# Kernel optimization log

Measured on AMD Instinct MI355X. Metric: run time of the kernel, lower is better.

Reference implementation:

```python
import jax, jax.numpy as jnp
import numpy as np
from jax.scipy.special import logsumexp

B, N, F_IN, HID = 8, 1024, 256, 128
RATIO = 0.5
NUM_LAYERS = 2
EPS_OT = 0.01  # forward default epsilon


def setup_inputs():
    key = jax.random.key(0)
    ks = jax.random.split(key, 6)
    x = jax.random.normal(ks[0], (B, N, F_IN), dtype=jnp.float32)
    adj = (jax.random.uniform(ks[1], (B, N, N)) < 0.02).astype(jnp.float32)
    adj = jnp.maximum(adj, jnp.swapaxes(adj, 1, 2))  # symmetric sparse-ish graph
    mask = jnp.ones((B, N), dtype=bool)
    W1 = jax.random.normal(ks[2], (F_IN, HID), dtype=jnp.float32) / np.sqrt(F_IN)
    b1 = jnp.zeros((HID,), dtype=jnp.float32)
    Watt = jax.random.normal(ks[3], (HID, 1), dtype=jnp.float32) / np.sqrt(HID)
    batt = jnp.zeros((1,), dtype=jnp.float32)
    W2 = jax.random.normal(ks[4], (HID, F_IN), dtype=jnp.float32) / np.sqrt(HID)
    b2 = jnp.zeros((F_IN,), dtype=jnp.float32)
    return dict(x=x, adj=adj, mask=mask, W1=W1, b1=b1, Watt=Watt, batt=batt,
                W2=W2, b2=b2, opt_epochs=20)


def _gcn_norm(adj):
    # DenseGCNConv add_loop + symmetric normalization
    n = adj.shape[-1]
    A = adj + jnp.eye(n, dtype=adj.dtype)
    d = jnp.maximum(A.sum(-1), 1.0) ** -0.5
    return d[..., :, None] * A * d[..., None, :]


def dense_gcn(x, adj, W, b, mask=None):
    out = jnp.einsum('bij,bjh->bih', _gcn_norm(adj), x @ W) + b
    if mask is not None:
        out = out * mask[..., None].astype(out.dtype)
    return out


def normalize_batch_adj(adj):
    # CoarsenBlock.normalize_batch_adj: self-loop sym-norm, zero-row masked
    n = adj.shape[-1]
    A = adj + jnp.eye(n, dtype=adj.dtype)
    d = jnp.maximum(A.sum(-1), 1.0) ** -0.5
    newA = d[..., :, None] * A * d[..., None, :]
    return (adj.sum(-1) > 0).astype(adj.dtype)[..., None] * newA


def coarsen_block(x, adj, Watt, batt):
    # attention score per node, squared then sigmoid  -> [B, N]
    alpha = jax.nn.sigmoid(dense_gcn(x, adj, Watt, batt) ** 2)[..., 0]
    norm_adj = normalize_batch_adj(adj)
    k = int(adj.shape[1] * RATIO) + 1
    cut = jax.lax.top_k(alpha, k)[0][:, -1]                 # per-sample k-th value
    cut_alpha = jax.nn.relu(alpha + 1e-7 - cut[:, None])    # soft top-k gate
    S = norm_adj * cut_alpha[:, None, :]
    S = S / jnp.maximum(jnp.abs(S).sum(-1, keepdims=True), 1e-12)  # row L1 norm
    emb = jnp.einsum('bij,bif->bjf', S, x)                  # S^T x
    tmp = jnp.einsum('bij,bik->bjk', S, adj)                # S^T adj
    new_adj = jnp.einsum('bjk,bkl->bjl', tmp, S)            # S^T adj S
    return emb, new_adj, S


def sinkhorn_loss(x, y, eps, niter):
    # squared-euclidean cost via gram trick (no [n,m,f] intermediate)
    C = (jnp.sum(x * x, -1)[:, None] + jnp.sum(y * y, -1)[None, :]
         - 2.0 * (x @ y.T))
    n, m = C.shape
    log_mu = jnp.full((n,), -np.log(n), dtype=C.dtype)
    log_nu = jnp.full((m,), -np.log(m), dtype=C.dtype)

    def M(u, v):
        return (-C + u[:, None] + v[None, :]) / eps

    def step(carry, _):
        u, v = carry
        u = eps * (log_mu - logsumexp(M(u, v), axis=1)) + u
        v = eps * (log_nu - logsumexp(M(u, v), axis=0)) + v
        return (u, v), None

    (u, v), _ = jax.lax.scan(step, (jnp.zeros_like(log_mu), jnp.zeros_like(log_nu)),
                             None, length=niter)
    pi = jnp.exp(M(u, v))
    return jnp.sum(pi * C)


def reference(x, adj, mask, W1, b1, Watt, batt, W2, b2, opt_epochs):
    x1 = jax.nn.relu(dense_gcn(x, adj, W1, b1, mask))
    xs0 = x1.mean(axis=1)
    new_adjs = [adj]
    Ss = []
    coarse_x, new_adj = x1, adj
    for _ in range(NUM_LAYERS):
        coarse_x, new_adj, S = coarsen_block(coarse_x, new_adj, Watt, batt)
        new_adjs.append(new_adj)
        Ss.append(S)
    x2 = dense_gcn(coarse_x, new_adj, W2, b2, mask)
    xs1 = x2.mean(axis=1)
    loss_fn = lambda a, b: sinkhorn_loss(a, b, EPS_OT, opt_epochs)
    opt_loss = jnp.sum(jax.vmap(loss_fn)(x, x2))
    return (xs0, xs1, new_adjs[0], new_adjs[1], new_adjs[2], Ss[0], Ss[1], opt_loss)
```

## Files before the change

kernel.cpp:

```cpp
#include <hip/hip_runtime.h>
#include <math.h>

#define BN   8
#define NN   1024
#define FIN  256
#define HIDN 128
#define KTOP 513
#define NITER 20
#define EPS_S 0.01f
#define INV_EPS 100.0f
#define LOG_MU (-6.9314718055994531f)
#define SNB 256
#define SENTU 0xFFFFFFFFu

typedef __attribute__((ext_vector_type(8))) short bfrag8;
typedef __attribute__((ext_vector_type(4))) float facc4;

#define GLOAD16(g, l) __builtin_amdgcn_global_load_lds( \
    (const __attribute__((address_space(1))) unsigned int*)(g), \
    (__attribute__((address_space(3))) unsigned int*)(l), 16, 0, 0)

static __device__ __forceinline__ float wred_sum(float s) {
#pragma unroll
  for (int o = 32; o > 0; o >>= 1) s += __shfl_xor(s, o);
  return s;
}
static __device__ __forceinline__ unsigned short f2b(float f) {
  unsigned int u = __float_as_uint(f);
  u += 0x7fff + ((u >> 16) & 1);
  return (unsigned short)(u >> 16);
}
static __device__ __forceinline__ float b2f(unsigned short h) {
  return __uint_as_float((unsigned int)h << 16);
}

template<int WRBF, int WCOPY>
__global__ __launch_bounds__(256) void k_rowstats4(const float* __restrict__ adj,
                                                   float* __restrict__ dv,
                                                   float* __restrict__ rm,
                                                   unsigned short* __restrict__ abf,
                                                   float* __restrict__ ocopy) {
  int r0 = blockIdx.x << 2;
  int t = threadIdx.x, lane = t & 63, wv = t >> 6;
  __shared__ float sm[4][4];
#pragma unroll
  for (int r = 0; r < 4; ++r) {
    float4 v = ((const float4*)(adj + (long)(r0 + r) * NN))[t];
    if (WRBF) {
      ushort4 h; h.x = f2b(v.x); h.y = f2b(v.y); h.z = f2b(v.z); h.w = f2b(v.w);
      *(ushort4*)(abf + (long)(r0 + r) * NN + t * 4) = h;
    }
    if (WCOPY) ((float4*)(ocopy + (long)(r0 + r) * NN))[t] = v;
    float s = (v.x + v.y) + (v.z + v.w);
    s = wred_sum(s);
    if (lane == 0) sm[wv][r] = s;
  }
  __syncthreads();
  if (t < 4) {
    float tot = sm[0][t] + sm[1][t] + sm[2][t] + sm[3][t];
    dv[r0 + t] = rsqrtf(fmaxf(tot + 1.0f, 1.0f));
    rm[r0 + t] = tot > 0.0f ? 1.0f : 0.0f;
  }
}

__global__ __launch_bounds__(256) void k_rowstats4b(
    const unsigned short* __restrict__ abf, float* __restrict__ dv,
    float* __restrict__ rm) {
  int r0 = blockIdx.x << 2;
  int t = threadIdx.x, lane = t & 63, wv = t >> 6;
  __shared__ float sm[4][4];
#pragma unroll
  for (int r = 0; r < 4; ++r) {
    ushort4 h = ((const ushort4*)(abf + (long)(r0 + r) * NN))[t];
    float s = (b2f(h.x) + b2f(h.y)) + (b2f(h.z) + b2f(h.w));
    s = wred_sum(s);
    if (lane == 0) sm[wv][r] = s;
  }
  __syncthreads();
  if (t < 4) {
    float tot = sm[0][t] + sm[1][t] + sm[2][t] + sm[3][t];
    dv[r0 + t] = rsqrtf(fmaxf(tot + 1.0f, 1.0f));
    rm[r0 + t] = tot > 0.0f ? 1.0f : 0.0f;
  }
}

__global__ __launch_bounds__(256) void k_f2b(const float* __restrict__ X,
                                             unsigned short* __restrict__ Y) {
  long i = ((long)blockIdx.x * 256 + threadIdx.x) * 4;
  float4 v = *(const float4*)(X + i);
  Y[i] = f2b(v.x); Y[i + 1] = f2b(v.y); Y[i + 2] = f2b(v.z); Y[i + 3] = f2b(v.w);
}

__global__ __launch_bounds__(256) void k_w1t(const float* __restrict__ W,
                                             unsigned short* __restrict__ Wt) {
  int idx = blockIdx.x * 256 + threadIdx.x;
  int n = idx >> 8, k = idx & 255;
  Wt[idx] = f2b(W[k * HIDN + n]);
}

__global__ __launch_bounds__(256) void k_prep2(
    const float* __restrict__ X0, const float* __restrict__ X1,
    unsigned short* __restrict__ Xh0, unsigned short* __restrict__ Xl0,
    unsigned short* __restrict__ Xh1, unsigned short* __restrict__ Xl1,
    float* __restrict__ sq0, float* __restrict__ sq1) {
  int bb = blockIdx.x;
  const float* X; unsigned short* Xh; unsigned short* Xl; float* sq; int rb;
  if (bb < 2048) { X = X0; Xh = Xh0; Xl = Xl0; sq = sq0; rb = bb; }
  else { X = X1; Xh = Xh1; Xl = Xl1; sq = sq1; rb = bb - 2048; }
  int t = threadIdx.x, lane = t & 63, wv = t >> 6;
  int row = rb * 4 + wv;
  long base = (long)row * FIN + lane * 4;
  float4 v = *(const float4*)(X + base);
  ushort4 h, l;
  h.x = f2b(v.x); l.x = f2b(v.x - b2f(h.x));
  h.y = f2b(v.y); l.y = f2b(v.y - b2f(h.y));
  h.z = f2b(v.z); l.z = f2b(v.z - b2f(h.z));
  h.w = f2b(v.w); l.w = f2b(v.w - b2f(h.w));
  *(ushort4*)(Xh + base) = h;
  *(ushort4*)(Xl + base) = l;
  float s = v.x * v.x + v.y * v.y + v.z * v.z + v.w * v.w;
  s = wred_sum(s);
  if (lane == 0) sq[row] = s;
}

__global__ __launch_bounds__(256) void k_transp(const float* __restrict__ X,
                                                unsigned short* __restrict__ Xt,
                                                int R, int C) {
  __shared__ float tile[64][65];
  long bb = blockIdx.z;
  const float* Xb = X + bb * (long)R * C;
  unsigned short* Xtb = Xt + bb * (long)R * C;
  int r0 = blockIdx.y * 64, c0 = blockIdx.x * 64;
  int t = threadIdx.x;
  int tr = t >> 4, tc4 = (t & 15) * 4;
#pragma unroll
  for (int p = 0; p < 4; ++p) {
    float4 v = *(const float4*)(Xb + (long)(r0 + tr + p * 16) * C + c0 + tc4);
    tile[tr + p * 16][tc4 + 0] = v.x; tile[tr + p * 16][tc4 + 1] = v.y;
    tile[tr + p * 16][tc4 + 2] = v.z; tile[tr + p * 16][tc4 + 3] = v.w;
  }
  __syncthreads();
  int jj = t >> 2, i0 = (t & 3) * 16;
  unsigned short* orow = Xtb + (long)(c0 + jj) * R + r0 + i0;
#pragma unroll
  for (int q = 0; q < 16; ++q) orow[q] = f2b(tile[i0 + q][jj]);
}

template<int SPLIT>
__global__ __launch_bounds__(256) void k_stc(const float* __restrict__ XW,
                                             const float* __restrict__ dvv,
                                             unsigned short* __restrict__ Bh,
                                             unsigned short* __restrict__ Bl,
                                             int F) {
  __shared__ float tile[64][65];
  __shared__ float dl[64];
  int bz = blockIdx.z;
  const float* Xb = XW + (long)bz * NN * F;
  int j0 = blockIdx.x * 64;
  int n0 = blockIdx.y * 64;
  int t = threadIdx.x;
  int tr = t >> 4, tc4 = (t & 15) * 4;
#pragma unroll
  for (int p = 0; p < 4; ++p) {
    float4 v = *(const float4*)(Xb + (long)(j0 + tr + p * 16) * F + n0 + tc4);
    tile[tr + p * 16][tc4 + 0] = v.x; tile[tr + p * 16][tc4 + 1] = v.y;
    tile[tr + p * 16][tc4 + 2] = v.z; tile[tr + p * 16][tc4 + 3] = v.w;
  }
  if (t < 64) dl[t] = dvv[(bz << 10) + j0 + t];
  __syncthreads();
  int nn = t >> 2, i0 = (t & 3) * 16;
  long obase = ((long)bz * F + n0 + nn) * NN + j0 + i0;
#pragma unroll
  for (int q = 0; q < 16; ++q) {
    float v = tile[i0 + q][nn] * dl[i0 + q];
    unsigned short h = f2b(v);
    Bh[obase + q] = h;
    if (SPLIT) Bl[obase + q] = f2b(v - b2f(h));
  }
}

template<int WF32, int WBF>
__global__ __launch_bounds__(256) void k_mfma_nt(
    const unsigned short* __restrict__ A, const unsigned short* __restrict__ B,
    float* __restrict__ Cf, unsigned short* __restrict__ Cb,
    unsigned short* __restrict__ Cb2,
    int K, int ldA, int ldB, int ldC, long sA, long sB, long sC) {
  __shared__ unsigned short As[128 * 32];
  __shared__ unsigned short Bs[128 * 32];
  int bz = blockIdx.z;
  A += bz * sA; B += bz * sB;
  int m0 = blockIdx.y * 128, n0 = blockIdx.x * 128;
  int tid = threadIdx.x, lane = tid & 63, w = tid >> 6;
  int wr = w >> 1, wc = w & 1;
  facc4 acc[4][4];
#pragma unroll
  for (int i = 0; i < 4; ++i)
#pragma unroll
    for (int j = 0; j < 4; ++j)
#pragma unroll
      for (int q = 0; q < 4; ++q) acc[i][j][q] = 0.f;

  int rA0 = w * 16 + (lane >> 2);
  int kslot = lane & 3;

  for (int k0 = 0; k0 < K; k0 += 32) {
#pragma unroll
    for (int i = 0; i < 2; ++i) {
      int row = i * 64 + rA0;
      int ks = (kslot ^ (row & 3)) << 3;
      GLOAD16(A + (long)(m0 + row) * ldA + k0 + ks, As + (i * 64 + w * 16) * 32);
      GLOAD16(B + (long)(n0 + row) * ldB + k0 + ks, Bs + (i * 64 + w * 16) * 32);
    }
    __syncthreads();
    bfrag8 af[4], bfr[4];
#pragma unroll
    for (int mi = 0; mi < 4; ++mi) {
      int row = wr * 64 + mi * 16 + (lane & 15);
      int sl = (((lane >> 4) ^ (row & 3)) << 3);
      af[mi] = *(const bfrag8*)(As + row * 32 + sl);
    }
#pragma unroll
    for (int ni = 0; ni < 4; ++ni) {
      int row = wc * 64 + ni * 16 + (lane & 15);
      int sl = (((lane >> 4) ^ (row & 3)) << 3);
      bfr[ni] = *(const bfrag8*)(Bs + row * 32 + sl);
    }
#pragma unroll
    for (int mi = 0; mi < 4; ++mi)
#pragma unroll
      for (int ni = 0; ni < 4; ++ni)
        acc[mi][ni] = __builtin_amdgcn_mfma_f32_16x16x32_bf16(
            af[mi], bfr[ni], acc[mi][ni], 0, 0, 0);
    __syncthreads();
  }
  if (WF32) Cf += bz * sC;
  if (WBF) Cb += bz * sC;
  if (WBF == 2) Cb2 += bz * sC;
#pragma unroll
  for (int mi = 0; mi < 4; ++mi) {
    int rowb = m0 + wr * 64 + mi * 16 + ((lane >> 4) << 2);
#pragma unroll
    for (int ni = 0; ni < 4; ++ni) {
      int col = n0 + wc * 64 + ni * 16 + (lane & 15);
#pragma unroll
      for (int q = 0; q < 4; ++q) {
        long off = (long)(rowb + q) * ldC + col;
        float v = acc[mi][ni][q];
        if (WF32) Cf[off] = v;
        if (WBF == 1) Cb[off] = f2b(v);
        if (WBF == 2) {
          unsigned short h = f2b(v);
          Cb[off] = h;
          Cb2[off] = f2b(v - b2f(h));
        }
      }
    }
  }
}

__global__ __launch_bounds__(256) void k_coars(
    const unsigned short* __restrict__ St, const unsigned short* __restrict__ Badj,
    const unsigned short* __restrict__ cxt,
    unsigned short* __restrict__ tmpo, float* __restrict__ embo) {
  __shared__ unsigned short As[128 * 32];
  __shared__ unsigned short Bs[128 * 32];
  int bz = blockIdx.z;
  int bx = blockIdx.x;
  int em = (bx == 8);
  const unsigned short* A = St + (long)bz * 1048576;
  const unsigned short* B = em ? (cxt + (long)bz * 131072)
                               : (Badj + (long)bz * 1048576);
  int m0 = blockIdx.y * 128, n0 = em ? 0 : bx * 128;
  int tid = threadIdx.x, lane = tid & 63, w = tid >> 6;
  int wr = w >> 1, wc = w & 1;
  facc4 acc[4][4];
#pragma unroll
  for (int i = 0; i < 4; ++i)
#pragma unroll
    for (int j = 0; j < 4; ++j)
#pragma unroll
      for (int q = 0; q < 4; ++q) acc[i][j][q] = 0.f;

  int rA0 = w * 16 + (lane >> 2);
  int kslot = lane & 3;

  for (int k0 = 0; k0 < NN; k0 += 32) {
#pragma unroll
    for (int i = 0; i < 2; ++i) {
      int row = i * 64 + rA0;
      int ks = (kslot ^ (row & 3)) << 3;
      GLOAD16(A + (long)(m0 + row) * NN + k0 + ks, As + (i * 64 + w * 16) * 32);
      GLOAD16(B + (long)(n0 + row) * NN + k0 + ks, Bs + (i * 64 + w * 16) * 32);
    }
    __syncthreads();
    bfrag8 af[4], bfr[4];
#pragma unroll
    for (int mi = 0; mi < 4; ++mi) {
      int row = wr * 64 + mi * 16 + (lane & 15);
      int sl = (((lane >> 4) ^ (row & 3)) << 3);
      af[mi] = *(const bfrag8*)(As + row * 32 + sl);
    }
#pragma unroll
    for (int ni = 0; ni < 4; ++ni) {
      int row = wc * 64 + ni * 16 + (lane & 15);
      int sl = (((lane >> 4) ^ (row & 3)) << 3);
      bfr[ni] = *(const bfrag8*)(Bs + row * 32 + sl);
    }
#pragma unroll
    for (int mi = 0; mi < 4; ++mi)
#pragma unroll
      for (int ni = 0; ni < 4; ++ni)
        acc[mi][ni] = __builtin_amdgcn_mfma_f32_16x16x32_bf16(
            af[mi], bfr[ni], acc[mi][ni], 0, 0, 0);
    __syncthreads();
  }
#pragma unroll
  for (int mi = 0; mi < 4; ++mi) {
    int rowb = m0 + wr * 64 + mi * 16 + ((lane >> 4) << 2);
#pragma unroll
    for (int ni = 0; ni < 4; ++ni) {
      int col = n0 + wc * 64 + ni * 16 + (lane & 15);
#pragma unroll
      for (int q = 0; q < 4; ++q) {
        float v = acc[mi][ni][q];
        if (em)
          embo[(long)bz * 131072 + (long)(rowb + q) * HIDN + col] = v;
        else
          tmpo[(long)bz * 1048576 + (long)(rowb + q) * NN + col] = f2b(v);
      }
    }
  }
}

template<int SPLIT, int RELU>
__global__ __launch_bounds__(256) void k_mfma_gcn(
    const unsigned short* __restrict__ Ah, const unsigned short* __restrict__ Al,
    const unsigned short* __restrict__ Bh, const unsigned short* __restrict__ Bl,
    const float* __restrict__ dvv, const float* __restrict__ XW,
    const float* __restrict__ bias, float* __restrict__ Cf, int F) {
  __shared__ unsigned short AsH[128 * 32], BsH[128 * 32];
  __shared__ unsigned short AsL[SPLIT ? 128 * 32 : 16], BsL[SPLIT ? 128 * 32 : 16];
  int bz = blockIdx.z;
  const unsigned short* Ahb = Ah + (long)bz * NN * NN;
  const unsigned short* Alb = SPLIT ? Al + (long)bz * NN * NN : nullptr;
  const unsigned short* Bhb = Bh + (long)bz * F * NN;
  const unsigned short* Blb = SPLIT ? Bl + (long)bz * F * NN : nullptr;
  int m0 = blockIdx.y * 128, n0 = blockIdx.x * 128;
  int tid = threadIdx.x, lane = tid & 63, w = tid >> 6;
  int wr = w >> 1, wc = w & 1;
  facc4 acc[4][4];
#pragma unroll
  for (int i = 0; i < 4; ++i)
#pragma unroll
    for (int j = 0; j < 4; ++j)
#pragma unroll
      for (int q = 0; q < 4; ++q) acc[i][j][q] = 0.f;

  int rA0 = w * 16 + (lane >> 2);
  int kslot = lane & 3;

  for (int k0 = 0; k0 < NN; k0 += 32) {
#pragma unroll
    for (int i = 0; i < 2; ++i) {
      int row = i * 64 + rA0;
      int ks = (kslot ^ (row & 3)) << 3;
      int ld = (i * 64 + w * 16) * 32;
      GLOAD16(Ahb + (long)(m0 + row) * NN + k0 + ks, AsH + ld);
      GLOAD16(Bhb + (long)(n0 + row) * NN + k0 + ks, BsH + ld);
      if (SPLIT) {
        GLOAD16(Alb + (long)(m0 + row) * NN + k0 + ks, AsL + ld);
        GLOAD16(Blb + (long)(n0 + row) * NN + k0 + ks, BsL + ld);
      }
    }
    __syncthreads();
    bfrag8 afh[4], bfh[4], afl[4], bfl[4];
#pragma unroll
    for (int mi = 0; mi < 4; ++mi) {
      int row = wr * 64 + mi * 16 + (lane & 15);
      int sl = (((lane >> 4) ^ (row & 3)) << 3);
      afh[mi] = *(const bfrag8*)(AsH + row * 32 + sl);
      if (SPLIT) afl[mi] = *(const bfrag8*)(AsL + row * 32 + sl);
    }
#pragma unroll
    for (int ni = 0; ni < 4; ++ni) {
      int row = wc * 64 + ni * 16 + (lane & 15);
      int sl = (((lane >> 4) ^ (row & 3)) << 3);
      bfh[ni] = *(const bfrag8*)(BsH + row * 32 + sl);
      if (SPLIT) bfl[ni] = *(const bfrag8*)(BsL + row * 32 + sl);
    }
#pragma unroll
    for (int mi = 0; mi < 4; ++mi)
#pragma unroll
      for (int ni = 0; ni < 4; ++ni) {
        acc[mi][ni] = __builtin_amdgcn_mfma_f32_16x16x32_bf16(
            afh[mi], bfh[ni], acc[mi][ni], 0, 0, 0);
        if (SPLIT) {
          acc[mi][ni] = __builtin_amdgcn_mfma_f32_16x16x32_bf16(
              afh[mi], bfl[ni], acc[mi][ni], 0, 0, 0);
          acc[mi][ni] = __builtin_amdgcn_mfma_f32_16x16x32_bf16(
              afl[mi], bfh[ni], acc[mi][ni], 0, 0, 0);
        }
      }
    __syncthreads();
  }
  Cf += (long)bz * NN * F;
#pragma unroll
  for (int mi = 0; mi < 4; ++mi) {
    int rowb = m0 + wr * 64 + mi * 16 + ((lane >> 4) << 2);
#pragma unroll
    for (int ni = 0; ni < 4; ++ni) {
      int col = n0 + wc * 64 + ni * 16 + (lane & 15);
      float bcol = bias[col];
#pragma unroll
      for (int q = 0; q < 4; ++q) {
        float dm = dvv[(bz << 10) + rowb + q];
        float xwv = XW[((long)(bz << 10) + rowb + q) * F + col];
        float v = dm * (acc[mi][ni][q] + dm * xwv) + bcol;
        if (RELU) v = fmaxf(v, 0.f);
        Cf[(long)(rowb + q) * F + col] = v;
      }
    }
  }
}

__global__ __launch_bounds__(256) void k_mfma_gram(
    const unsigned short* __restrict__ Ah, const unsigned short* __restrict__ Al,
    const unsigned short* __restrict__ Bh, const unsigned short* __restrict__ Bl,
    const float* __restrict__ xx, const float* __restrict__ yy,
    float* __restrict__ Cf, float* __restrict__ Ct) {
  __shared__ unsigned short AsH[128 * 32], AsL[128 * 32];
  __shared__ unsigned short BsH[128 * 32], BsL[128 * 32];
  int bz = blockIdx.z;
  long boff = (long)bz * NN * FIN;
  Ah += boff; Al += boff; Bh += boff; Bl += boff;
  const float* xxb = xx + (bz << 10);
  const float* yyb = yy + (bz << 10);
  int m0 = blockIdx.y * 128, n0 = blockIdx.x * 128;
  int tid = threadIdx.x, lane = tid & 63, w = tid >> 6;
  int wr = w >> 1, wc = w & 1;
  facc4 acc[4][4];
#pragma unroll
  for (int i = 0; i < 4; ++i)
#pragma unroll
    for (int j = 0; j < 4; ++j)
#pragma unroll
      for (int q = 0; q < 4; ++q) acc[i][j][q] = 0.f;

  int rA0 = w * 16 + (lane >> 2);
  int kslot = lane & 3;

  for (int k0 = 0; k0 < FIN; k0 += 32) {
#pragma unroll
    for (int i = 0; i < 2; ++i) {
      int row = i * 64 + rA0;
      int ks = (kslot ^ (row & 3)) << 3;
      long ga = (long)(m0 + row) * FIN + k0 + ks;
      long gb = (long)(n0 + row) * FIN + k0 + ks;
      int ld = (i * 64 + w * 16) * 32;
      GLOAD16(Ah + ga, AsH + ld);
      GLOAD16(Al + ga, AsL + ld);
      GLOAD16(Bh + gb, BsH + ld);
      GLOAD16(Bl + gb, BsL + ld);
    }
    __syncthreads();
    bfrag8 afh[4], afl[4], bfh[4], bfl[4];
#pragma unroll
    for (int mi = 0; mi < 4; ++mi) {
      int row = wr * 64 + mi * 16 + (lane & 15);
      int sl = (((lane >> 4) ^ (row & 3)) << 3);
      afh[mi] = *(const bfrag8*)(AsH + row * 32 + sl);
      afl[mi] = *(const bfrag8*)(AsL + row * 32 + sl);
    }
#pragma unroll
    for (int ni = 0; ni < 4; ++ni) {
      int row = wc * 64 + ni * 16 + (lane & 15);
      int sl = (((lane >> 4) ^ (row & 3)) << 3);
      bfh[ni] = *(const bfrag8*)(BsH + row * 32 + sl);
      bfl[ni] = *(const bfrag8*)(BsL + row * 32 + sl);
    }
#pragma unroll
    for (int mi = 0; mi < 4; ++mi)
#pragma unroll
      for (int ni = 0; ni < 4; ++ni) {
        acc[mi][ni] = __builtin_amdgcn_mfma_f32_16x16x32_bf16(
            afh[mi], bfh[ni], acc[mi][ni], 0, 0, 0);
        acc[mi][ni] = __builtin_amdgcn_mfma_f32_16x16x32_bf16(
            afh[mi], bfl[ni], acc[mi][ni], 0, 0, 0);
        acc[mi][ni] = __builtin_amdgcn_mfma_f32_16x16x32_bf16(
            afl[mi], bfh[ni], acc[mi][ni], 0, 0, 0);
      }
    __syncthreads();
  }
  Cf += (long)bz * NN * NN;
  Ct += (long)bz * NN * NN;
#pragma unroll
  for (int mi = 0; mi < 4; ++mi) {
    int rowb = m0 + wr * 64 + mi * 16 + ((lane >> 4) << 2);
#pragma unroll
    for (int ni = 0; ni < 4; ++ni) {
      int col = n0 + wc * 64 + ni * 16 + (lane & 15);
      float yv = yyb[col];
      float4 tv;
#pragma unroll
      for (int q = 0; q < 4; ++q) {
        float v = xxb[rowb + q] + yv - 2.f * acc[mi][ni][q];
        Cf[(long)(rowb + q) * NN + col] = v;
        ((float*)&tv)[q] = v;
      }
      *(float4*)(Ct + (long)col * NN + rowb) = tv;
    }
  }
}

__global__ __launch_bounds__(256) void k_rowdot(const float* __restrict__ X,
                                                const float* __restrict__ w,
                                                float* __restrict__ out) {
  int t = threadIdx.x; int lane = t & 63; int wv = t >> 6;
  int row = blockIdx.x * 4 + wv;
  const float* xr = X + (long)row * HIDN;
  float s = xr[lane] * w[lane] + xr[lane + 64] * w[lane + 64];
  s = wred_sum(s);
  if (lane == 0) out[row] = s;
}

__global__ __launch_bounds__(256) void k_alpha4b(const unsigned short* __restrict__ adj,
                                                 const float* __restrict__ dv,
                                                 const float* __restrict__ s0,
                                                 const float* __restrict__ batt,
                                                 float* __restrict__ alpha) {
  int r0 = blockIdx.x << 2; int b = r0 >> 10; int i0 = r0 & (NN - 1);
  int t = threadIdx.x, lane = t & 63, wv = t >> 6;
  float4 d4 = ((const float4*)(dv + (b << 10)))[t];
  float4 s4 = ((const float4*)(s0 + (b << 10)))[t];
  float w4[4];
  w4[0] = d4.x * s4.x; w4[1] = d4.y * s4.y; w4[2] = d4.z * s4.z; w4[3] = d4.w * s4.w;
  __shared__ float sm[4][4];
#pragma unroll
  for (int r = 0; r < 4; ++r) {
    ushort4 h = ((const ushort4*)(adj + (long)(r0 + r) * NN))[t];
    float dot = b2f(h.x) * w4[0] + b2f(h.y) * w4[1] +
                b2f(h.z) * w4[2] + b2f(h.w) * w4[3];
    int i = i0 + r;
    if ((i >> 2) == t) dot += w4[i & 3];
    dot = wred_sum(dot);
    if (lane == 0) sm[wv][r] = dot;
  }
  __syncthreads();
  if (t < 4) {
    float dot = sm[0][t] + sm[1][t] + sm[2][t] + sm[3][t];
    float tt = dv[r0 + t] * dot + batt[0];
    alpha[r0 + t] = 1.f / (1.f + __expf(-tt * tt));
  }
}

__global__ __launch_bounds__(512) void k_topk(const float* __restrict__ alpha,
                                              float* __restrict__ cut) {
  __shared__ float smv[NN];
  int b = blockIdx.x; int t = threadIdx.x;
  smv[t] = alpha[(b << 10) + t];
  smv[t + 512] = alpha[(b << 10) + t + 512];
  __syncthreads();
  for (int k2 = 2; k2 <= NN; k2 <<= 1) {
    for (int j2 = k2 >> 1; j2 > 0; j2 >>= 1) {
      int i = ((t / j2) * (j2 << 1)) + (t % j2);
      int ixj = i + j2;
      bool up = ((i & k2) == 0);
      float a = smv[i], c = smv[ixj];
      if ((a > c) == up) { smv[i] = c; smv[ixj] = a; }
      __syncthreads();
    }
  }
  if (t == 0) cut[b] = smv[NN - KTOP];
}

__global__ __launch_bounds__(256) void k_sbuild4b(const unsigned short* __restrict__ adj,
                                                  const float* __restrict__ dv,
                                                  const float* __restrict__ rm,
                                                  const float* __restrict__ alpha,
                                                  const float* __restrict__ cut,
                                                  float* __restrict__ S) {
  int r0 = blockIdx.x << 2; int b = r0 >> 10; int i0 = r0 & (NN - 1);
  int t = threadIdx.x, lane = t & 63, wv = t >> 6;
  float cb = cut[b];
  float4 d4 = ((const float4*)(dv + (b << 10)))[t];
  float4 al4 = ((const float4*)(alpha + (b << 10)))[t];
  float4 dg;
  dg.x = d4.x * fmaxf(al4.x + 1e-7f - cb, 0.f);
  dg.y = d4.y * fmaxf(al4.y + 1e-7f - cb, 0.f);
  dg.z = d4.z * fmaxf(al4.z + 1e-7f - cb, 0.f);
  dg.w = d4.w * fmaxf(al4.w + 1e-7f - cb, 0.f);
  __shared__ float sm[4][4];
  __shared__ float sinv[4];
  float4 vals[4];
#pragma unroll
  for (int r = 0; r < 4; ++r) {
    float di = dv[r0 + r] * rm[r0 + r];
    ushort4 h = ((const ushort4*)(adj + (long)(r0 + r) * NN))[t];
    float4 a4;
    a4.x = b2f(h.x); a4.y = b2f(h.y); a4.z = b2f(h.z); a4.w = b2f(h.w);
    int i = i0 + r;
    if ((i >> 2) == t) ((float*)&a4)[i & 3] += 1.f;
    vals[r].x = di * dg.x * a4.x; vals[r].y = di * dg.y * a4.y;
    vals[r].z = di * dg.z * a4.z; vals[r].w = di * dg.w * a4.w;
    float s = (fabsf(vals[r].x) + fabsf(vals[r].y)) +
              (fabsf(vals[r].z) + fabsf(vals[r].w));
    s = wred_sum(s);
    if (lane == 0) sm[wv][r] = s;
  }
  __syncthreads();
  if (t < 4) sinv[t] = 1.f / fmaxf(sm[0][t] + sm[1][t] + sm[2][t] + sm[3][t], 1e-12f);
  __syncthreads();
#pragma unroll
  for (int r = 0; r < 4; ++r) {
    float inv = sinv[r];
    float4 o; o.x = vals[r].x * inv; o.y = vals[r].y * inv;
    o.z = vals[r].z * inv; o.w = vals[r].w * inv;
    ((float4*)(S + (long)(r0 + r) * NN))[t] = o;
  }
}

template<int GCN>
__global__ __launch_bounds__(256) void k_gemm_ks(
    const float* __restrict__ A, const float* __restrict__ Bm, float* __restrict__ P,
    int M, int Nn, int K, int KS, long sA, long sB,
    const float* __restrict__ dv) {
  __shared__ float As[8][132];
  __shared__ float Bs[8][132];
  int z = blockIdx.z;
  int b = z / KS, ks = z % KS;
  int KC = K / KS;
  A += (long)b * sA; Bm += (long)b * sB;
  const float* dvb = GCN ? (dv + (long)b * NN) : nullptr;
  int m0 = blockIdx.y * 128, n0 = blockIdx.x * 128;
  int tid = threadIdx.x;
  int tx = tid & 15, ty = tid >> 4;
  float acc[8][8];
#pragma unroll
  for (int i = 0; i < 8; i++)
#pragma unroll
    for (int j = 0; j < 8; j++) acc[i][j] = 0.f;

  float drow = 0.f;
  if (GCN) drow = dvb[m0 + (tid >> 1)];

  for (int k0 = ks * KC; k0 < ks * KC + KC; k0 += 8) {
    {
      int r = tid >> 1, c4 = (tid & 1) * 4;
      float4 av = *(const float4*)(A + (long)(m0 + r) * K + k0 + c4);
      float a4[4] = {av.x, av.y, av.z, av.w};
      if (GCN) {
#pragma unroll
        for (int q = 0; q < 4; ++q) {
          int gj = k0 + c4 + q;
          float val = a4[q] + ((m0 + r) == gj ? 1.f : 0.f);
          a4[q] = drow * dvb[gj] * val;
        }
      }
      As[c4 + 0][r] = a4[0]; As[c4 + 1][r] = a4[1];
      As[c4 + 2][r] = a4[2]; As[c4 + 3][r] = a4[3];
    }
    {
      int kr = tid >> 5, c4 = (tid & 31) * 4;
      float4 bv = *(const float4*)(Bm + (long)(k0 + kr) * Nn + n0 + c4);
      *(float4*)&Bs[kr][c4] = bv;
    }
    __syncthreads();
#pragma unroll
    for (int k = 0; k < 8; ++k) {
      float av[8], bv[8];
      *(float4*)&av[0] = *(const float4*)&As[k][ty * 8];
      *(float4*)&av[4] = *(const float4*)&As[k][ty * 8 + 4];
      *(float4*)&bv[0] = *(const float4*)&Bs[k][tx * 8];
      *(float4*)&bv[4] = *(const float4*)&Bs[k][tx * 8 + 4];
#pragma unroll
      for (int i = 0; i < 8; i++)
#pragma unroll
        for (int j = 0; j < 8; j++)
          acc[i][j] = fmaf(av[i], bv[j], acc[i][j]);
    }
    __syncthreads();
  }
  float* Pz = P + (long)z * M * Nn;
#pragma unroll
  for (int i = 0; i < 8; ++i) {
    int m = m0 + ty * 8 + i;
    float* prow = Pz + (long)m * Nn + n0 + tx * 8;
    *(float4*)&prow[0] = *(float4*)&acc[i][0];
    *(float4*)&prow[4] = *(float4*)&acc[i][4];
  }
}

template<int RELU, int BIAS>
__global__ __launch_bounds__(256) void k_red_bias(
    const float* __restrict__ P, const float* __restrict__ bias,
    float* __restrict__ out, int Nn, int KS, long chunk) {
  long u = ((long)blockIdx.x * 256 + threadIdx.x) * 4;
  long b = u / chunk; long rem = u % chunk;
  const float* p = P + b * KS * chunk + rem;
  float4 s = *(const float4*)p;
  for (int k = 1; k < KS; ++k) {
    float4 q = *(const float4*)(p + (long)k * chunk);
    s.x += q.x; s.y += q.y; s.z += q.z; s.w += q.w;
  }
  if (BIAS) {
    int n = (int)(rem % Nn);
    s.x += bias[n]; s.y += bias[n + 1]; s.z += bias[n + 2]; s.w += bias[n + 3];
  }
  if (RELU) {
    s.x = fmaxf(s.x, 0.f); s.y = fmaxf(s.y, 0.f);
    s.z = fmaxf(s.z, 0.f); s.w = fmaxf(s.w, 0.f);
  }
  *(float4*)(out + u) = s;
}

__global__ __launch_bounds__(256) void k_colmean(const float* __restrict__ X, int Fd,
                                                 float* __restrict__ out) {
  int nb = Fd >> 6;
  int b = blockIdx.x / nb; int f0 = (blockIdx.x % nb) << 6;
  int t = threadIdx.x;
  int f = f0 + (t & 63); int rc = t >> 6;
  const float* xb = X + (long)b * NN * Fd;
  float s = 0.f;
  for (int i = rc * 256; i < rc * 256 + 256; ++i) s += xb[(long)i * Fd + f];
  __shared__ float sm[256];
  sm[t] = s; __syncthreads();
  if (t < 64) out[b * Fd + f] = (sm[t] + sm[t + 64] + sm[t + 128] + sm[t + 192]) * (1.f / NN);
}


static __device__ __forceinline__ float2 load_cohere2(const float* p) {
  float2 v;
  asm volatile("global_load_dwordx2 %0, %1, off sc0 sc1\n\ts_waitcnt vmcnt(0)"
               : "=v"(v) : "v"(p) : "memory");
  return v;
}
static __device__ __forceinline__ float load_cohere1(const float* p) {
  float v;
  asm volatile("global_load_dword %0, %1, off sc0 sc1\n\ts_waitcnt vmcnt(0)"
               : "=v"(v) : "v"(p) : "memory");
  return v;
}
static __device__ __forceinline__ void store_cohere1(float* p, float v) {
  asm volatile("global_store_dword %0, %1, off sc0 sc1\n\ts_waitcnt vmcnt(0)"
               :: "v"(p), "v"(v) : "memory");
}

static __device__ __forceinline__ void pollstage(const float* __restrict__ src,
                                                 float* __restrict__ vls, int t) {
  float2 v; int spin = 0;
  for (;;) {
    v = load_cohere2(src + t * 2);
    if ((__float_as_uint(v.x) != SENTU) & (__float_as_uint(v.y) != SENTU)) break;
    if (++spin > (1 << 20)) break;
    __builtin_amdgcn_s_sleep(1);
  }
  __syncthreads();
  *(float2*)(vls + t * 2) = v;
  __syncthreads();
}

template<int LOSS, int STORE>
static __device__ __forceinline__ void pass_reg(const float4 (&Cr)[16],
    const float* __restrict__ vls, float* __restrict__ dbout,
    int jc, int row, float* __restrict__ lossacc, float& mxs, int fresh) {
  float4 vr[16];
#pragma unroll
  for (int k = 0; k < 16; ++k)
    vr[k] = *(const float4*)(vls + (k * 16 + jc) * 4);
  float mx = mxs;
  if (fresh) {
    float m0 = -3.0e38f, m1 = m0, m2 = m0, m3 = m0;
#pragma unroll
    for (int k = 0; k < 16; ++k) {
      m0 = fmaxf(m0, vr[k].x - Cr[k].x);
      m1 = fmaxf(m1, vr[k].y - Cr[k].y);
      m2 = fmaxf(m2, vr[k].z - Cr[k].z);
      m3 = fmaxf(m3, vr[k].w - Cr[k].w);
    }
    mx = fmaxf(fmaxf(m0, m1), fmaxf(m2, m3));
#pragma unroll
    for (int m = 1; m <= 8; m <<= 1) mx = fmaxf(mx, __shfl_xor(mx, m));
  }
  float ls, ld = 0.f;
  {
    float s0 = 0, s1 = 0, s2 = 0, s3 = 0, d0 = 0, d1 = 0, d2 = 0, d3 = 0;
#pragma unroll
    for (int k = 0; k < 16; ++k) {
      float e0 = __expf(vr[k].x - Cr[k].x - mx);
      float e1 = __expf(vr[k].y - Cr[k].y - mx);
      float e2 = __expf(vr[k].z - Cr[k].z - mx);
      float e3 = __expf(vr[k].w - Cr[k].w - mx);
      s0 += e0; s1 += e1; s2 += e2; s3 += e3;
      if (LOSS) {
        d0 = fmaf(e0, Cr[k].x, d0); d1 = fmaf(e1, Cr[k].y, d1);
        d2 = fmaf(e2, Cr[k].z, d2); d3 = fmaf(e3, Cr[k].w, d3);
      }
    }
    ls = (s0 + s1) + (s2 + s3);
    if (LOSS) ld = (d0 + d1) + (d2 + d3);
  }
#pragma unroll
  for (int m = 1; m <= 8; m <<= 1) {
    ls += __shfl_xor(ls, m);
    if (LOSS) ld += __shfl_xor(ld, m);
  }
  if (!(ls > 1e-25f && ls < 1e25f)) {
    float m0 = -3.0e38f, m1 = m0, m2 = m0, m3 = m0;
#pragma unroll
    for (int k = 0; k < 16; ++k) {
      m0 = fmaxf(m0, vr[k].x - Cr[k].x);
      m1 = fmaxf(m1, vr[k].y - Cr[k].y);
      m2 = fmaxf(m2, vr[k].z - Cr[k].z);
      m3 = fmaxf(m3, vr[k].w - Cr[k].w);
    }
    mx = fmaxf(fmaxf(m0, m1), fmaxf(m2, m3));
#pragma unroll
    for (int m = 1; m <= 8; m <<= 1) mx = fmaxf(mx, __shfl_xor(mx, m));
    float s0 = 0, s1 = 0, s2 = 0, s3 = 0, d0 = 0, d1 = 0, d2 = 0, d3 = 0;
#pragma unroll
    for (int k = 0; k < 16; ++k) {
      float e0 = __expf(vr[k].x - Cr[k].x - mx);
      float e1 = __expf(vr[k].y - Cr[k].y - mx);
      float e2 = __expf(vr[k].z - Cr[k].z - mx);
      float e3 = __expf(vr[k].w - Cr[k].w - mx);
      s0 += e0; s1 += e1; s2 += e2; s3 += e3;
      if (LOSS) {
        d0 = fmaf(e0, Cr[k].x, d0); d1 = fmaf(e1, Cr[k].y, d1);
        d2 = fmaf(e2, Cr[k].z, d2); d3 = fmaf(e3, Cr[k].w, d3);
      }
    }
    ls = (s0 + s1) + (s2 + s3);
    if (LOSS) ld = (d0 + d1) + (d2 + d3);
#pragma unroll
    for (int m = 1; m <= 8; m <<= 1) {
      ls += __shfl_xor(ls, m);
      if (LOSS) ld += __shfl_xor(ld, m);
    }
  }
  mxs = mx;
  if (jc == 0) {
    float uval = LOG_MU - (mx + __logf(ls));
    if (STORE) store_cohere1(dbout + row, uval);
    if (LOSS) *lossacc += (ld / ls) * (1.0f / 1024.0f);
  }
}

__global__ __launch_bounds__(512, 1) void k_sink_reg(
    const float* __restrict__ Cm, const float* __restrict__ Ct,
    float* __restrict__ db, float* __restrict__ part,
    float* __restrict__ oloss) {
  int bid = blockIdx.x, t = threadIdx.x, lane = t & 63, wvi = t >> 6;
  int jc = lane & 15;
  int grp = bid & 7;
  int inner = bid >> 3;
  int row = (grp << 10) + inner * 32 + wvi * 4 + (lane >> 4);
  __shared__ float vls[1024];
  float4 Creg[16], Ctreg[16];
  {
    const float4* cp = (const float4*)(Cm + (long)row * NN);
    const float4* tp = (const float4*)(Ct + (long)row * NN);
#pragma unroll
    for (int k = 0; k < 16; ++k) {
      float4 c = cp[k * 16 + jc], ct = tp[k * 16 + jc];
      Creg[k].x = c.x * INV_EPS;  Creg[k].y = c.y * INV_EPS;
      Creg[k].z = c.z * INV_EPS;  Creg[k].w = c.w * INV_EPS;
      Ctreg[k].x = ct.x * INV_EPS; Ctreg[k].y = ct.y * INV_EPS;
      Ctreg[k].z = ct.z * INV_EPS; Ctreg[k].w = ct.w * INV_EPS;
    }
  }
  {
    float2 v = *(const float2*)(db + (grp << 10) + t * 2);
    *(float2*)(vls + t * 2) = v;
  }
  __syncthreads();
  float lossacc = 0.f;
  float mxu = 0.f, mxv = 0.f;
  int g = 1;
  for (int it = 0; it < NITER; ++it) {
    pass_reg<0, 1>(Creg, vls, db + (long)g * 8192, jc, row, nullptr, mxu, it == 0);
    pollstage(db + (long)g * 8192 + (grp << 10), vls, t);
    ++g;
    if (it < NITER - 1) {
      pass_reg<0, 1>(Ctreg, vls, db + (long)g * 8192, jc, row, nullptr, mxv, it == 0);
      pollstage(db + (long)g * 8192 + (grp << 10), vls, t);
      ++g;
    } else {
      pass_reg<1, 0>(Ctreg, vls, nullptr, jc, row, &lossacc, mxv, 0);
    }
  }
  float s = wred_sum(lossacc);
  __shared__ float lsm[8];
  if (lane == 0) lsm[wvi] = s;
  __syncthreads();
  if (t == 0) {
    float ps = 0.f;
#pragma unroll
    for (int i = 0; i < 8; ++i) ps += lsm[i];
    store_cohere1(part + bid, ps);
  }
  if (bid == 0) {
    float s2 = 0.f;
    if (t < SNB) {
      int spin = 0;
      for (;;) {
        s2 = load_cohere1(part + t);
        if (__float_as_uint(s2) != SENTU) break;
        if (++spin > (1 << 20)) { s2 = 0.f; break; }
        __builtin_amdgcn_s_sleep(1);
      }
    }
    s2 = wred_sum(s2);
    __shared__ float sm2[8];
    if (lane == 0) sm2[wvi] = s2;
    __syncthreads();
    if (t == 0) {
      float tot = 0.f;
#pragma unroll
      for (int i = 0; i < 8; ++i) tot += sm2[i];
      oloss[0] = tot * EPS_S;
    }
  }
}

extern "C" void kernel_launch(void* const* d_in, const int* in_sizes, int n_in,
                              void* d_out, int out_size, void* d_ws, size_t ws_size,
                              hipStream_t stream) {
  const float* x    = (const float*)d_in[0];
  const float* adj  = (const float*)d_in[1];
  const float* W1   = (const float*)d_in[3];
  const float* b1   = (const float*)d_in[4];
  const float* Watt = (const float*)d_in[5];
  const float* batt = (const float*)d_in[6];
  const float* W2   = (const float*)d_in[7];
  const float* b2   = (const float*)d_in[8];

  float* out = (float*)d_out;
  float* xs0   = out;
  float* xs1   = out + 1024;
  float* oadj0 = out + 3072;
  float* oadj1 = oadj0 + 8388608;
  float* oadj2 = oadj1 + 8388608;
  float* oS0   = oadj2 + 8388608;
  float* oS1   = oS0 + 8388608;
  float* oloss = oS1 + 8388608;

  float* ws   = (float*)d_ws;
  float* wXW  = ws;
  float* wCXA = wXW + 2097152;
  float* wCXB = wCXA + 1048576;
  float* wR   = wCXB + 1048576;
  float* wX2  = wR + 8388608;
  float* wStf = wX2 + 2097152;
  float* wCxtf= wStf + 4194304;
  float* wCt  = wCxtf + 524288;
  float* smb  = wCt + 8388608;

  unsigned short* tmp_bf = (unsigned short*)wR;
  unsigned short* a2h    = (unsigned short*)wCt;
  unsigned short* a2l    = a2h + 8388608;
  unsigned short* adj_bf = (unsigned short*)oadj2;
  unsigned short* St     = (unsigned short*)wStf;
  unsigned short* cxt    = (unsigned short*)wCxtf;
  unsigned short* x_bf   = (unsigned short*)wStf;
  unsigned short* Bg1    = (unsigned short*)wCxtf;
  unsigned short* Bg2h   = (unsigned short*)wStf;
  unsigned short* Bg2l   = (unsigned short*)(wStf + 2097152);
  unsigned short* xh  = (unsigned short*)wStf;
  unsigned short* xl  = xh + 2097152;
  unsigned short* x2h = xh + 4194304;
  unsigned short* x2l = xh + 6291456;
  float* Cmat = wR;
  float* d0 = smb;            float* rm0 = smb + 8192;
  float* d1 = smb + 16384;    float* rm1 = smb + 24576;
  float* d2 = smb + 32768;    float* rm2 = smb + 40960;
  float* s0v = smb + 49152;   float* alp = smb + 57344;
  float* xxv = smb + 65536;   float* yyv = smb + 73728;
  float* cutv = smb + 98304;  float* part = smb + 98368;
  unsigned short* W1t = (unsigned short*)(smb + 98624);
  float* db = smb + 131072;

  hipMemsetAsync(db, 0, (size_t)8192 * 4, stream);
  hipMemsetAsync(db + 8192, 0xFF, (size_t)40 * 8192 * 4, stream);
  hipMemsetAsync(part, 0xFF, (size_t)256 * 4, stream);

  k_rowstats4<1, 1><<<2048, 256, 0, stream>>>(adj, d0, rm0, adj_bf, oadj0);

  k_f2b<<<2048, 256, 0, stream>>>(x, x_bf);
  k_w1t<<<128, 256, 0, stream>>>(W1, W1t);
  k_mfma_nt<1, 0><<<dim3(1, 64, 1), 256, 0, stream>>>(x_bf, W1t, wXW, nullptr,
      nullptr, 256, 256, 256, 128, 0L, 0L, 0L);
  k_stc<0><<<dim3(16, 2, 8), 256, 0, stream>>>(wXW, d0, Bg1, nullptr, HIDN);
  k_mfma_gcn<0, 1><<<dim3(1, 8, 8), 256, 0, stream>>>(adj_bf, nullptr, Bg1,
      nullptr, d0, wXW, b1, wCXA, HIDN);
  k_colmean<<<16, 256, 0, stream>>>(wCXA, HIDN, xs0);

  k_rowdot<<<2048, 256, 0, stream>>>(wCXA, Watt, s0v);
  k_alpha4b<<<2048, 256, 0, stream>>>(adj_bf, d0, s0v, batt, alp);
  k_topk<<<8, 512, 0, stream>>>(alp, cutv);
  k_sbuild4b<<<2048, 256, 0, stream>>>(adj_bf, d0, rm0, alp, cutv, oS0);
  k_transp<<<dim3(16, 16, 8), 256, 0, stream>>>(oS0, St, 1024, 1024);
  k_transp<<<dim3(2, 16, 8), 256, 0, stream>>>(wCXA, cxt, 1024, 128);
  k_coars<<<dim3(9, 8, 8), 256, 0, stream>>>(St, adj_bf, cxt, tmp_bf, wCXB);
  k_mfma_nt<1, 1><<<dim3(8, 8, 8), 256, 0, stream>>>(tmp_bf, St, oadj1, adj_bf,
      nullptr, 1024, 1024, 1024, 1024, 1048576L, 1048576L, 1048576L);
  k_rowstats4b<<<2048, 256, 0, stream>>>(adj_bf, d1, rm1);

  k_rowdot<<<2048, 256, 0, stream>>>(wCXB, Watt, s0v);
  k_alpha4b<<<2048, 256, 0, stream>>>(adj_bf, d1, s0v, batt, alp);
  k_topk<<<8, 512, 0, stream>>>(alp, cutv);
  k_sbuild4b<<<2048, 256, 0, stream>>>(adj_bf, d1, rm1, alp, cutv, oS1);
  k_transp<<<dim3(16, 16, 8), 256, 0, stream>>>(oS1, St, 1024, 1024);
  k_transp<<<dim3(2, 16, 8), 256, 0, stream>>>(wCXB, cxt, 1024, 128);
  k_coars<<<dim3(9, 8, 8), 256, 0, stream>>>(St, adj_bf, cxt, tmp_bf, wCXA);
  k_mfma_nt<1, 2><<<dim3(8, 8, 8), 256, 0, stream>>>(tmp_bf, St, oadj2, a2h,
      a2l, 1024, 1024, 1024, 1024, 1048576L, 1048576L, 1048576L);
  k_rowstats4<0, 0><<<2048, 256, 0, stream>>>(oadj2, d2, rm2, nullptr, nullptr);

  k_gemm_ks<0><<<dim3(2, 64, 2), 256, 0, stream>>>(wCXA, W2, wR, 8192, FIN, HIDN,
      2, 0L, 0L, nullptr);
  k_red_bias<0, 0><<<2048, 256, 0, stream>>>(wR, nullptr, wXW, FIN, 2, 2097152L);
  k_stc<1><<<dim3(16, 4, 8), 256, 0, stream>>>(wXW, d2, Bg2h, Bg2l, FIN);
  k_mfma_gcn<1, 0><<<dim3(2, 8, 8), 256, 0, stream>>>(a2h, a2l, Bg2h, Bg2l,
      d2, wXW, b2, wX2, FIN);
  k_colmean<<<32, 256, 0, stream>>>(wX2, FIN, xs1);

  k_prep2<<<4096, 256, 0, stream>>>(x, wX2, xh, xl, x2h, x2l, xxv, yyv);
  k_mfma_gram<<<dim3(8, 8, 8), 256, 0, stream>>>(xh, xl, x2h, x2l, xxv, yyv,
      Cmat, wCt);
  k_sink_reg<<<SNB, 512, 0, stream>>>(Cmat, wCt, db, part, oloss);
}
```

Baseline: 750.0 us.

## Fuse adjacency row sums into GEMM epilogue, radix-select top-k, relax Sinkhorn store wait

Row sums of the coarsened adjacency are now accumulated in the MFMA GEMM epilogue through shared and global atomics, replacing two full-matrix rowstats passes with a tiny per-element kernel. The bitonic sort in top-k is replaced by a four-pass 8-bit radix select over float bit patterns, which is valid because alpha is positive. The Sinkhorn u store no longer waits on vmcnt after each store. The fused row sums are taken from fp32 accumulators rather than bf16-rounded values, so degrees can differ slightly, and dropping the store wait may affect cross-block coherence ordering.

```diff
diff --git a/kernel.cpp b/kernel.cpp
--- a/kernel.cpp
+++ b/kernel.cpp
@@ -63,25 +63,13 @@
   }
 }
 
-__global__ __launch_bounds__(256) void k_rowstats4b(
-    const unsigned short* __restrict__ abf, float* __restrict__ dv,
-    float* __restrict__ rm) {
-  int r0 = blockIdx.x << 2;
-  int t = threadIdx.x, lane = t & 63, wv = t >> 6;
-  __shared__ float sm[4][4];
-#pragma unroll
-  for (int r = 0; r < 4; ++r) {
-    ushort4 h = ((const ushort4*)(abf + (long)(r0 + r) * NN))[t];
-    float s = (b2f(h.x) + b2f(h.y)) + (b2f(h.z) + b2f(h.w));
-    s = wred_sum(s);
-    if (lane == 0) sm[wv][r] = s;
-  }
-  __syncthreads();
-  if (t < 4) {
-    float tot = sm[0][t] + sm[1][t] + sm[2][t] + sm[3][t];
-    dv[r0 + t] = rsqrtf(fmaxf(tot + 1.0f, 1.0f));
-    rm[r0 + t] = tot > 0.0f ? 1.0f : 0.0f;
-  }
+__global__ __launch_bounds__(256) void k_dfrom(const float* __restrict__ rs,
+                                               float* __restrict__ dv,
+                                               float* __restrict__ rm) {
+  int i = blockIdx.x * 256 + threadIdx.x;
+  float tot = rs[i];
+  dv[i] = rsqrtf(fmaxf(tot + 1.0f, 1.0f));
+  rm[i] = tot > 0.0f ? 1.0f : 0.0f;
 }
 
 __global__ __launch_bounds__(256) void k_f2b(const float* __restrict__ X,
@@ -179,14 +167,16 @@
   }
 }
 
-template<int WF32, int WBF>
+template<int WF32, int WBF, int RS>
 __global__ __launch_bounds__(256) void k_mfma_nt(
     const unsigned short* __restrict__ A, const unsigned short* __restrict__ B,
     float* __restrict__ Cf, unsigned short* __restrict__ Cb,
     unsigned short* __restrict__ Cb2,
-    int K, int ldA, int ldB, int ldC, long sA, long sB, long sC) {
+    int K, int ldA, int ldB, int ldC, long sA, long sB, long sC,
+    float* __restrict__ RSp) {
   __shared__ unsigned short As[128 * 32];
   __shared__ unsigned short Bs[128 * 32];
+  __shared__ float rsum[RS ? 128 : 4];
   int bz = blockIdx.z;
   A += bz * sA; B += bz * sB;
   int m0 = blockIdx.y * 128, n0 = blockIdx.x * 128;
@@ -233,6 +223,10 @@
             af[mi], bfr[ni], acc[mi][ni], 0, 0, 0);
     __syncthreads();
   }
+  if (RS) {
+    if (tid < 128) rsum[tid] = 0.f;
+    __syncthreads();
+  }
   if (WF32) Cf += bz * sC;
   if (WBF) Cb += bz * sC;
   if (WBF == 2) Cb2 += bz * sC;
@@ -240,10 +234,11 @@
   for (int mi = 0; mi < 4; ++mi) {
     int rowb = m0 + wr * 64 + mi * 16 + ((lane >> 4) << 2);
 #pragma unroll
-    for (int ni = 0; ni < 4; ++ni) {
-      int col = n0 + wc * 64 + ni * 16 + (lane & 15);
-#pragma unroll
-      for (int q = 0; q < 4; ++q) {
+    for (int q = 0; q < 4; ++q) {
+      float rp = 0.f;
+#pragma unroll
+      for (int ni = 0; ni < 4; ++ni) {
+        int col = n0 + wc * 64 + ni * 16 + (lane & 15);
         long off = (long)(rowb + q) * ldC + col;
         float v = acc[mi][ni][q];
         if (WF32) Cf[off] = v;
@@ -253,8 +248,19 @@
           Cb[off] = h;
           Cb2[off] = f2b(v - b2f(h));
         }
-      }
-    }
+        if (RS) rp += v;
+      }
+      if (RS) {
+        rp += __shfl_xor(rp, 1); rp += __shfl_xor(rp, 2);
+        rp += __shfl_xor(rp, 4); rp += __shfl_xor(rp, 8);
+        if ((lane & 15) == 0)
+          atomicAdd(&rsum[rowb + q - m0], rp);
+      }
+    }
+  }
+  if (RS) {
+    __syncthreads();
+    if (tid < 128) atomicAdd(&RSp[(long)bz * NN + m0 + tid], rsum[tid]);
   }
 }
 
@@ -555,22 +561,45 @@
 
 __global__ __launch_bounds__(512) void k_topk(const float* __restrict__ alpha,
                                               float* __restrict__ cut) {
-  __shared__ float smv[NN];
-  int b = blockIdx.x; int t = threadIdx.x;
-  smv[t] = alpha[(b << 10) + t];
-  smv[t + 512] = alpha[(b << 10) + t + 512];
+  int b = blockIdx.x, t = threadIdx.x;
+  unsigned e0 = __float_as_uint(alpha[(b << 10) + t]);
+  unsigned e1 = __float_as_uint(alpha[(b << 10) + t + 512]);
+  __shared__ int hist[256];
+  __shared__ unsigned pref;
+  __shared__ int kk;
+  if (t == 0) { pref = 0u; kk = KTOP; }
   __syncthreads();
-  for (int k2 = 2; k2 <= NN; k2 <<= 1) {
-    for (int j2 = k2 >> 1; j2 > 0; j2 >>= 1) {
-      int i = ((t / j2) * (j2 << 1)) + (t % j2);
-      int ixj = i + j2;
-      bool up = ((i & k2) == 0);
-      float a = smv[i], c = smv[ixj];
-      if ((a > c) == up) { smv[i] = c; smv[ixj] = a; }
-      __syncthreads();
-    }
-  }
-  if (t == 0) cut[b] = smv[NN - KTOP];
+  for (int pass = 0; pass < 4; ++pass) {
+    int shift = 24 - pass * 8;
+    if (t < 256) hist[t] = 0;
+    __syncthreads();
+    unsigned p = pref; int k = kk;
+    if (pass == 0 || (e0 >> (shift + 8)) == p)
+      atomicAdd(&hist[(e0 >> shift) & 255], 1);
+    if (pass == 0 || (e1 >> (shift + 8)) == p)
+      atomicAdd(&hist[(e1 >> shift) & 255], 1);
+    __syncthreads();
+    if (t < 64) {
+      int h0 = hist[4 * t], h1 = hist[4 * t + 1];
+      int h2 = hist[4 * t + 2], h3 = hist[4 * t + 3];
+      int s3 = h3, s2 = h2 + s3, s1 = h1 + s2, s0 = h0 + s1;
+      int T = s0, tin = T;
+#pragma unroll
+      for (int off = 1; off < 64; off <<= 1) {
+        int v = __shfl_down(tin, off);
+        if (t + off < 64) tin += v;
+      }
+      int above = tin - T;
+      int suf0 = s0 + above, suf1 = s1 + above;
+      int suf2 = s2 + above, suf3 = s3 + above, sufN = above;
+      if (suf0 >= k && suf1 < k) { pref = (p << 8) | (unsigned)(4 * t + 0); kk = k - suf1; }
+      if (suf1 >= k && suf2 < k) { pref = (p << 8) | (unsigned)(4 * t + 1); kk = k - suf2; }
+      if (suf2 >= k && suf3 < k) { pref = (p << 8) | (unsigned)(4 * t + 2); kk = k - suf3; }
+      if (suf3 >= k && sufN < k) { pref = (p << 8) | (unsigned)(4 * t + 3); kk = k - sufN; }
+    }
+    __syncthreads();
+  }
+  if (t == 0) cut[b] = __uint_as_float(pref);
 }
 
 __global__ __launch_bounds__(256) void k_sbuild4b(const unsigned short* __restrict__ adj,
@@ -740,6 +769,10 @@
                : "=v"(v) : "v"(p) : "memory");
   return v;
 }
+static __device__ __forceinline__ void dstore_ff(float* p, float v) {
+  asm volatile("global_store_dword %0, %1, off sc0 sc1"
+               :: "v"(p), "v"(v) : "memory");
+}
 static __device__ __forceinline__ void store_cohere1(float* p, float v) {
   asm volatile("global_store_dword %0, %1, off sc0 sc1\n\ts_waitcnt vmcnt(0)"
                :: "v"(p), "v"(v) : "memory");
@@ -840,7 +873,7 @@
   mxs = mx;
   if (jc == 0) {
     float uval = LOG_MU - (mx + __logf(ls));
-    if (STORE) store_cohere1(dbout + row, uval);
+    if (STORE) dstore_ff(dbout + row, uval);
     if (LOSS) *lossacc += (ld / ls) * (1.0f / 1024.0f);
   }
 }
@@ -978,17 +1011,20 @@
   float* cutv = smb + 98304;  float* part = smb + 98368;
   unsigned short* W1t = (unsigned short*)(smb + 98624);
   float* db = smb + 131072;
+  float* rowsum1 = smb + 131072 + 41 * 8192;
+  float* rowsum2 = rowsum1 + 8192;
 
   hipMemsetAsync(db, 0, (size_t)8192 * 4, stream);
   hipMemsetAsync(db + 8192, 0xFF, (size_t)40 * 8192 * 4, stream);
   hipMemsetAsync(part, 0xFF, (size_t)256 * 4, stream);
+  hipMemsetAsync(rowsum1, 0, (size_t)16384 * 4, stream);
 
   k_rowstats4<1, 1><<<2048, 256, 0, stream>>>(adj, d0, rm0, adj_bf, oadj0);
 
   k_f2b<<<2048, 256, 0, stream>>>(x, x_bf);
   k_w1t<<<128, 256, 0, stream>>>(W1, W1t);
-  k_mfma_nt<1, 0><<<dim3(1, 64, 1), 256, 0, stream>>>(x_bf, W1t, wXW, nullptr,
-      nullptr, 256, 256, 256, 128, 0L, 0L, 0L);
+  k_mfma_nt<1, 0, 0><<<dim3(1, 64, 1), 256, 0, stream>>>(x_bf, W1t, wXW, nullptr,
+      nullptr, 256, 256, 256, 128, 0L, 0L, 0L, nullptr);
   k_stc<0><<<dim3(16, 2, 8), 256, 0, stream>>>(wXW, d0, Bg1, nullptr, HIDN);
   k_mfma_gcn<0, 1><<<dim3(1, 8, 8), 256, 0, stream>>>(adj_bf, nullptr, Bg1,
       nullptr, d0, wXW, b1, wCXA, HIDN);
@@ -1001,9 +1037,9 @@
   k_transp<<<dim3(16, 16, 8), 256, 0, stream>>>(oS0, St, 1024, 1024);
   k_transp<<<dim3(2, 16, 8), 256, 0, stream>>>(wCXA, cxt, 1024, 128);
   k_coars<<<dim3(9, 8, 8), 256, 0, stream>>>(St, adj_bf, cxt, tmp_bf, wCXB);
-  k_mfma_nt<1, 1><<<dim3(8, 8, 8), 256, 0, stream>>>(tmp_bf, St, oadj1, adj_bf,
-      nullptr, 1024, 1024, 1024, 1024, 1048576L, 1048576L, 1048576L);
-  k_rowstats4b<<<2048, 256, 0, stream>>>(adj_bf, d1, rm1);
+  k_mfma_nt<1, 1, 1><<<dim3(8, 8, 8), 256, 0, stream>>>(tmp_bf, St, oadj1, adj_bf,
+      nullptr, 1024, 1024, 1024, 1024, 1048576L, 1048576L, 1048576L, rowsum1);
+  k_dfrom<<<32, 256, 0, stream>>>(rowsum1, d1, rm1);
 
   k_rowdot<<<2048, 256, 0, stream>>>(wCXB, Watt, s0v);
   k_alpha4b<<<2048, 256, 0, stream>>>(adj_bf, d1, s0v, batt, alp);
@@ -1012,9 +1048,9 @@
   k_transp<<<dim3(16, 16, 8), 256, 0, stream>>>(oS1, St, 1024, 1024);
   k_transp<<<dim3(2, 16, 8), 256, 0, stream>>>(wCXB, cxt, 1024, 128);
   k_coars<<<dim3(9, 8, 8), 256, 0, stream>>>(St, adj_bf, cxt, tmp_bf, wCXA);
-  k_mfma_nt<1, 2><<<dim3(8, 8, 8), 256, 0, stream>>>(tmp_bf, St, oadj2, a2h,
-      a2l, 1024, 1024, 1024, 1024, 1048576L, 1048576L, 1048576L);
-  k_rowstats4<0, 0><<<2048, 256, 0, stream>>>(oadj2, d2, rm2, nullptr, nullptr);
+  k_mfma_nt<1, 2, 1><<<dim3(8, 8, 8), 256, 0, stream>>>(tmp_bf, St, oadj2, a2h,
+      a2l, 1024, 1024, 1024, 1024, 1048576L, 1048576L, 1048576L, rowsum2);
+  k_dfrom<<<32, 256, 0, stream>>>(rowsum2, d2, rm2);
 
   k_gemm_ks<0><<<dim3(2, 64, 2), 256, 0, stream>>>(wCXA, W2, wR, 8192, FIN, HIDN,
       2, 0L, 0L, nullptr);
```

Measured after the change: 778.0 us. 1.04x slower.
